# Performance work log

Hardware: AMD Instinct MI355X
Metric: run time of the kernel (lower is better)

The kernel has to match this reference:

```python
import jax, jax.numpy as jnp
import numpy as np

N_GROUPS = 8
TOPK = 8
ROUTE_SCALE = 2.5


def _gate(x, weight, bias):
    # scores: [N, E] via router linear, sigmoid score_func
    scores = jax.nn.sigmoid(x @ weight.T + bias)
    original_scores = scores
    n = x.shape[0]
    g = scores.reshape(n, N_GROUPS, -1)              # [N, G, E/G]
    # bias is not None -> group score = sum of top-2 expert scores per group
    top2, _ = jax.lax.top_k(g, 2)                    # [N, G, 2]
    group_scores = top2.sum(axis=-1)                 # [N, G]
    topk_groups = TOPK // N_GROUPS                   # = 1
    _, gidx = jax.lax.top_k(group_scores, topk_groups)   # [N, topk_groups]
    keep = jnp.zeros((n, N_GROUPS), dtype=bool).at[
        jnp.arange(n)[:, None], gidx].set(True)      # selected groups
    masked = jnp.where(keep[:, :, None], g, -jnp.inf).reshape(n, -1)  # [N, E]
    _, idx = jax.lax.top_k(masked, TOPK)             # [N, TOPK]
    w = jnp.take_along_axis(original_scores, idx, axis=1)
    w = w / w.sum(axis=-1, keepdims=True)            # sigmoid -> renormalize
    w = (w * ROUTE_SCALE).astype(x.dtype)
    return w, idx


def setup_inputs() -> dict:
    key = jax.random.key(0)
    kx, kw, kb = jax.random.split(key, 3)
    x = jax.random.normal(kx, (8192, 7168), dtype=jnp.float32)
    weight = jax.random.normal(kw, (256, 7168), dtype=jnp.float32) * 0.02
    bias = jax.random.normal(kb, (256,), dtype=jnp.float32) * 0.02
    return {"x": x, "weight": weight, "bias": bias}


def reference(x, weight, bias):
    return _gate(x, weight, bias)
```

## Files before the change

kernel.cpp:

```cpp
#include <hip/hip_runtime.h>
#include <math.h>

#define M 8192
#define N 256
#define K 7168
#define KH 3584
#define N_GROUPS 8
#define TOPK 8
#define ROUTE_SCALE 2.5f

#define BM 64
#define BN 128
#define BK 64

typedef _Float16 half8 __attribute__((ext_vector_type(8)));
typedef _Float16 half4 __attribute__((ext_vector_type(4)));
typedef float f32x4 __attribute__((ext_vector_type(4)));

__device__ __forceinline__ void gload_lds16(const void* g, void* l) {
    __builtin_amdgcn_global_load_lds(
        (const __attribute__((address_space(1))) unsigned int*)g,
        (__attribute__((address_space(3))) unsigned int*)l,
        16, 0, 0);
}

__global__ __launch_bounds__(256) void convert_w(
        const float* __restrict__ W, _Float16* __restrict__ Wh,
        _Float16* __restrict__ Wl) {
    const int idx = blockIdx.x * 256 + threadIdx.x;
    const float4 w = ((const float4*)W)[idx];
    const float e[4] = {w.x, w.y, w.z, w.w};
    half4 h, l;
#pragma unroll
    for (int j = 0; j < 4; ++j) {
        const _Float16 hv = (_Float16)e[j];
        h[j] = hv;
        l[j] = (_Float16)(e[j] - (float)hv);
    }
    ((half4*)Wh)[idx] = h;
    ((half4*)Wl)[idx] = l;
}

__global__ __launch_bounds__(256, 2) void gemm_split(
        const float* __restrict__ X,
        const _Float16* __restrict__ Wh,
        const _Float16* __restrict__ Wl,
        float* __restrict__ P0,
        float* __restrict__ P1) {
    __shared__ _Float16 Ah[BM][BK], Al[BM][BK];
    __shared__ _Float16 Bh[BN][BK], Bl[BN][BK];

    const int tid = threadIdx.x;
    const int bid = blockIdx.x;
    const int xs = bid & 7;
    const int q = xs >> 1;
    const int nb = q & 1, ks = q >> 1;
    const int mb = ((bid >> 3) << 1) | (xs & 1);
    const int m0 = mb * BM, n0 = nb * BN, kb = ks * KH;

    const int lane = tid & 63, wave = tid >> 6;
    const int wr = wave >> 1, wc = wave & 1;
    const int lrow = lane & 15, lkq = lane >> 4;

    const int blr = lane >> 3;
    const int bcsw = (lane & 7) ^ blr;

    const int ar = tid >> 2;
    const int ac0 = (tid & 3) << 1;

    f32x4 acc[2][4];
#pragma unroll
    for (int i = 0; i < 2; ++i)
#pragma unroll
        for (int j = 0; j < 4; ++j) acc[i][j] = (f32x4){0.f, 0.f, 0.f, 0.f};

    const float* Abase = X + (size_t)(m0 + ar) * K + kb + ac0 * 8;
    const _Float16* Whb = Wh + kb + bcsw * 8;
    const _Float16* Wlb = Wl + kb + bcsw * 8;

    for (int k0 = 0; k0 < KH; k0 += BK) {
        __syncthreads();
#pragma unroll
        for (int i = 0; i < 4; ++i) {
            const int r8 = wave * 4 + i;
            const int lr = r8 * 8 + blr;
            const size_t go = (size_t)(n0 + lr) * K + k0;
            gload_lds16(Whb + go, &Bh[r8 * 8][0]);
            gload_lds16(Wlb + go, &Bl[r8 * 8][0]);
        }
        const float* ga = Abase + k0;
        float4 f[4];
#pragma unroll
        for (int i = 0; i < 4; ++i) f[i] = ((const float4*)ga)[i];
#pragma unroll
        for (int c = 0; c < 2; ++c) {
            const float e[8] = {f[c*2].x, f[c*2].y, f[c*2].z, f[c*2].w,
                                f[c*2+1].x, f[c*2+1].y, f[c*2+1].z, f[c*2+1].w};
            half8 h, l;
#pragma unroll
            for (int j = 0; j < 8; ++j) {
                const _Float16 hv = (_Float16)e[j];
                h[j] = hv;
                l[j] = (_Float16)(e[j] - (float)hv);
            }
            const int p = (ac0 + c) ^ (ar & 7);
            *(half8*)&Ah[ar][p * 8] = h;
            *(half8*)&Al[ar][p * 8] = l;
        }
        __syncthreads();

#pragma unroll
        for (int s = 0; s < 2; ++s) {
            const int pc8 = ((s * 4 + lkq) ^ (lrow & 7)) * 8;
            const half8 ah0 = *(const half8*)&Ah[wr*32 + lrow][pc8];
            const half8 ah1 = *(const half8*)&Ah[wr*32 + 16 + lrow][pc8];
            const half8 al0 = *(const half8*)&Al[wr*32 + lrow][pc8];
            const half8 al1 = *(const half8*)&Al[wr*32 + 16 + lrow][pc8];
#pragma unroll
            for (int j = 0; j < 4; ++j) {
                const int br = wc*64 + j*16 + lrow;
                const half8 bh = *(const half8*)&Bh[br][pc8];
                const half8 bl = *(const half8*)&Bl[br][pc8];
                acc[0][j] = __builtin_amdgcn_mfma_f32_16x16x32_f16(ah0, bh, acc[0][j], 0, 0, 0);
                acc[1][j] = __builtin_amdgcn_mfma_f32_16x16x32_f16(ah1, bh, acc[1][j], 0, 0, 0);
                acc[0][j] = __builtin_amdgcn_mfma_f32_16x16x32_f16(ah0, bl, acc[0][j], 0, 0, 0);
                acc[1][j] = __builtin_amdgcn_mfma_f32_16x16x32_f16(ah1, bl, acc[1][j], 0, 0, 0);
                acc[0][j] = __builtin_amdgcn_mfma_f32_16x16x32_f16(al0, bh, acc[0][j], 0, 0, 0);
                acc[1][j] = __builtin_amdgcn_mfma_f32_16x16x32_f16(al1, bh, acc[1][j], 0, 0, 0);
            }
        }
    }

    float* P = ks ? P1 : P0;
#pragma unroll
    for (int i = 0; i < 2; ++i) {
        const int row = m0 + wr * 32 + i * 16 + lkq * 4;
#pragma unroll
        for (int j = 0; j < 4; ++j) {
            const int col = n0 + wc * 64 + j * 16 + lrow;
#pragma unroll
            for (int r = 0; r < 4; ++r)
                P[(size_t)(row + r) * N + col] = acc[i][j][r];
        }
    }
}

__global__ __launch_bounds__(256) void gate_topk(
        const float* __restrict__ P0, const float* __restrict__ P1,
        const float* __restrict__ bias,
        float* __restrict__ out_w, float* __restrict__ out_i) {
    const int row = blockIdx.x * 4 + (threadIdx.x >> 6);
    const int lane = threadIdx.x & 63;

    const float4 a4 = *reinterpret_cast<const float4*>(P0 + (size_t)row * N + lane * 4);
    const float4 b4 = *reinterpret_cast<const float4*>(P1 + (size_t)row * N + lane * 4);
    const float4 bb = *reinterpret_cast<const float4*>(bias + lane * 4);
    float v[4] = {1.f / (1.f + expf(-(a4.x + b4.x + bb.x))),
                  1.f / (1.f + expf(-(a4.y + b4.y + bb.y))),
                  1.f / (1.f + expf(-(a4.z + b4.z + bb.z))),
                  1.f / (1.f + expf(-(a4.w + b4.w + bb.w)))};

    float t1 = v[0], t2 = -1.f;
#pragma unroll
    for (int j = 1; j < 4; ++j) {
        if (v[j] > t1) { t2 = t1; t1 = v[j]; }
        else if (v[j] > t2) { t2 = v[j]; }
    }
#pragma unroll
    for (int m = 1; m <= 4; m <<= 1) {
        const float o1 = __shfl_xor(t1, m, 64);
        const float o2 = __shfl_xor(t2, m, 64);
        const float n1 = fmaxf(t1, o1);
        const float n2 = fmaxf(fminf(t1, o1), fmaxf(t2, o2));
        t1 = n1; t2 = n2;
    }
    float gs = t1 + t2;
    int gid = lane >> 3;
#pragma unroll
    for (int m = 8; m <= 32; m <<= 1) {
        const float og = __shfl_xor(gs, m, 64);
        const int oi = __shfl_xor(gid, m, 64);
        if (og > gs || (og == gs && oi < gid)) { gs = og; gid = oi; }
    }

    const bool inG = ((lane >> 3) == gid);
    if (!inG) { v[0] = v[1] = v[2] = v[3] = -1.f; }

    float wv[8];
    int wi[8];
#pragma unroll
    for (int r = 0; r < 8; ++r) {
        float bv = v[0]; int bj = 0;
#pragma unroll
        for (int j = 1; j < 4; ++j)
            if (v[j] > bv) { bv = v[j]; bj = j; }
        int be = lane * 4 + bj;
#pragma unroll
        for (int m = 1; m <= 32; m <<= 1) {
            const float ov = __shfl_xor(bv, m, 64);
            const int oe = __shfl_xor(be, m, 64);
            if (ov > bv || (ov == bv && oe < be)) { bv = ov; be = oe; }
        }
        wv[r] = bv; wi[r] = be;
        if ((be >> 2) == lane) v[be & 3] = -1.f;
    }

    float sum = 0.f;
#pragma unroll
    for (int r = 0; r < 8; ++r) sum += wv[r];

    if (lane == 0) {
#pragma unroll
        for (int r = 0; r < 8; ++r) {
            out_w[(size_t)row * TOPK + r] = wv[r] / sum * ROUTE_SCALE;
            out_i[(size_t)row * TOPK + r] = (float)wi[r];
        }
    }
}

extern "C" void kernel_launch(void* const* d_in, const int* in_sizes, int n_in,
                              void* d_out, int out_size, void* d_ws, size_t ws_size,
                              hipStream_t stream) {
    const float* x = (const float*)d_in[0];
    const float* w = (const float*)d_in[1];
    const float* b = (const float*)d_in[2];

    char* ws = (char*)d_ws;
    _Float16* Wh = (_Float16*)ws;
    _Float16* Wl = (_Float16*)(ws + 3670016);
    float* P0 = (float*)(ws + 7340032);
    float* P1 = (float*)(ws + 7340032 + 8388608);

    float* out_w = (float*)d_out;
    float* out_i = out_w + (size_t)M * TOPK;

    convert_w<<<(N * K / 4) / 256, 256, 0, stream>>>(w, Wh, Wl);
    gemm_split<<<512, 256, 0, stream>>>(x, Wh, Wl, P0, P1);
    gate_topk<<<M / 4, 256, 0, stream>>>(P0, P1, b, out_w, out_i);
}
```

Measured before the change: 401.4 us.

## Use three-way split-K with atomic accumulation into a single partial buffer

The GEMM moves from a 2-way split-K with two partial buffers to a 3-way split-K (38/37/37 k-steps) that atomically adds into one zero-initialised buffer. The grid grows from 512 to 768 blocks and launch bounds allow 3 blocks per SM, aiming to fill the 256 CUs more evenly and cut tail imbalance. This adds a zeroing kernel and float atomics on output, which make the sum order nondeterministic. The top-k kernel now reads one buffer instead of two.

```diff
diff --git a/kernel.cpp b/kernel.cpp
--- a/kernel.cpp
+++ b/kernel.cpp
@@ -4,7 +4,6 @@
 #define M 8192
 #define N 256
 #define K 7168
-#define KH 3584
 #define N_GROUPS 8
 #define TOPK 8
 #define ROUTE_SCALE 2.5f
@@ -22,6 +21,10 @@
         (const __attribute__((address_space(1))) unsigned int*)g,
         (__attribute__((address_space(3))) unsigned int*)l,
         16, 0, 0);
+}
+
+__global__ __launch_bounds__(256) void zero_p(float4* __restrict__ P) {
+    P[blockIdx.x * 256 + threadIdx.x] = float4{0.f, 0.f, 0.f, 0.f};
 }
 
 __global__ __launch_bounds__(256) void convert_w(
@@ -41,22 +44,24 @@
     ((half4*)Wl)[idx] = l;
 }
 
-__global__ __launch_bounds__(256, 2) void gemm_split(
+__global__ __launch_bounds__(256, 3) void gemm_split(
         const float* __restrict__ X,
         const _Float16* __restrict__ Wh,
         const _Float16* __restrict__ Wl,
-        float* __restrict__ P0,
-        float* __restrict__ P1) {
+        float* __restrict__ P) {
     __shared__ _Float16 Ah[BM][BK], Al[BM][BK];
     __shared__ _Float16 Bh[BN][BK], Bl[BN][BK];
 
     const int tid = threadIdx.x;
     const int bid = blockIdx.x;
-    const int xs = bid & 7;
-    const int q = xs >> 1;
-    const int nb = q & 1, ks = q >> 1;
-    const int mb = ((bid >> 3) << 1) | (xs & 1);
-    const int m0 = mb * BM, n0 = nb * BN, kb = ks * KH;
+    const int x3 = bid & 7;
+    const int nb = (bid >> 3) & 1;
+    const int r = bid >> 4;
+    const int ks = r % 3;
+    const int mb = ((r / 3) << 3) | x3;
+    const int m0 = mb * BM, n0 = nb * BN;
+    const int kstart = (ks == 0) ? 0 : (ks == 1 ? 38 : 75);
+    const int nsteps = (ks == 0) ? 38 : 37;
 
     const int lane = tid & 63, wave = tid >> 6;
     const int wr = wave >> 1, wc = wave & 1;
@@ -74,11 +79,12 @@
 #pragma unroll
         for (int j = 0; j < 4; ++j) acc[i][j] = (f32x4){0.f, 0.f, 0.f, 0.f};
 
-    const float* Abase = X + (size_t)(m0 + ar) * K + kb + ac0 * 8;
-    const _Float16* Whb = Wh + kb + bcsw * 8;
-    const _Float16* Wlb = Wl + kb + bcsw * 8;
-
-    for (int k0 = 0; k0 < KH; k0 += BK) {
+    const float* Abase = X + (size_t)(m0 + ar) * K + ac0 * 8;
+    const _Float16* Whb = Wh + bcsw * 8;
+    const _Float16* Wlb = Wl + bcsw * 8;
+
+    for (int t = 0; t < nsteps; ++t) {
+        const int k0 = (kstart + t) * BK;
         __syncthreads();
 #pragma unroll
         for (int i = 0; i < 4; ++i) {
@@ -131,7 +137,6 @@
         }
     }
 
-    float* P = ks ? P1 : P0;
 #pragma unroll
     for (int i = 0; i < 2; ++i) {
         const int row = m0 + wr * 32 + i * 16 + lkq * 4;
@@ -139,26 +144,24 @@
         for (int j = 0; j < 4; ++j) {
             const int col = n0 + wc * 64 + j * 16 + lrow;
 #pragma unroll
-            for (int r = 0; r < 4; ++r)
-                P[(size_t)(row + r) * N + col] = acc[i][j][r];
+            for (int rr = 0; rr < 4; ++rr)
+                atomicAdd(&P[(size_t)(row + rr) * N + col], acc[i][j][rr]);
         }
     }
 }
 
 __global__ __launch_bounds__(256) void gate_topk(
-        const float* __restrict__ P0, const float* __restrict__ P1,
-        const float* __restrict__ bias,
+        const float* __restrict__ P, const float* __restrict__ bias,
         float* __restrict__ out_w, float* __restrict__ out_i) {
     const int row = blockIdx.x * 4 + (threadIdx.x >> 6);
     const int lane = threadIdx.x & 63;
 
-    const float4 a4 = *reinterpret_cast<const float4*>(P0 + (size_t)row * N + lane * 4);
-    const float4 b4 = *reinterpret_cast<const float4*>(P1 + (size_t)row * N + lane * 4);
+    const float4 a4 = *reinterpret_cast<const float4*>(P + (size_t)row * N + lane * 4);
     const float4 bb = *reinterpret_cast<const float4*>(bias + lane * 4);
-    float v[4] = {1.f / (1.f + expf(-(a4.x + b4.x + bb.x))),
-                  1.f / (1.f + expf(-(a4.y + b4.y + bb.y))),
-                  1.f / (1.f + expf(-(a4.z + b4.z + bb.z))),
-                  1.f / (1.f + expf(-(a4.w + b4.w + bb.w)))};
+    float v[4] = {1.f / (1.f + expf(-(a4.x + bb.x))),
+                  1.f / (1.f + expf(-(a4.y + bb.y))),
+                  1.f / (1.f + expf(-(a4.z + bb.z))),
+                  1.f / (1.f + expf(-(a4.w + bb.w)))};
 
     float t1 = v[0], t2 = -1.f;
 #pragma unroll
@@ -228,13 +231,13 @@
     char* ws = (char*)d_ws;
     _Float16* Wh = (_Float16*)ws;
     _Float16* Wl = (_Float16*)(ws + 3670016);
-    float* P0 = (float*)(ws + 7340032);
-    float* P1 = (float*)(ws + 7340032 + 8388608);
+    float* P = (float*)(ws + 7340032);
 
     float* out_w = (float*)d_out;
     float* out_i = out_w + (size_t)M * TOPK;
 
+    zero_p<<<(M * N / 4) / 256, 256, 0, stream>>>((float4*)P);
     convert_w<<<(N * K / 4) / 256, 256, 0, stream>>>(w, Wh, Wl);
-    gemm_split<<<512, 256, 0, stream>>>(x, Wh, Wl, P0, P1);
-    gate_topk<<<M / 4, 256, 0, stream>>>(P0, P1, b, out_w, out_i);
-}
+    gemm_split<<<768, 256, 0, stream>>>(x, Wh, Wl, P);
+    gate_topk<<<M / 4, 256, 0, stream>>>(P, b, out_w, out_i);
+}
```

Result: no change. 402.0 us (+0.1%).
